# Kernel optimization log

Measured on AMD Instinct MI355X. Metric: run time of the kernel, lower is better.

The kernel has to match this reference:

```python
import jax, jax.numpy as jnp
import numpy as np

B, S, D, H, BLK, R = 2, 4096, 768, 12, 64, 3
NB = S // BLK  # 64 blocks
HD = D // H    # 64 head dim


def layer_norm(x, g, b, eps=1e-6):
    m = jnp.mean(x, -1, keepdims=True)
    v = jnp.mean((x - m) ** 2, -1, keepdims=True)
    return (x - m) / jnp.sqrt(v + eps) * g + b


def bigbird_attention(x, wq, bq, wk, bk, wv, bv, wo, bo, rand_attn):
    # x: [B,S,D]; rand_attn: [H, NB-2, R] int block indices
    def heads(t):
        return t.reshape(B, S, H, HD).transpose(0, 2, 1, 3)  # [B,H,S,HD]
    q = heads(x @ wq + bq)
    k = heads(x @ wk + bk)
    v = heads(x @ wv + bv)
    scale = 1.0 / jnp.sqrt(jnp.asarray(HD, x.dtype))

    qb = q.reshape(B, H, NB, BLK, HD)
    kb = k.reshape(B, H, NB, BLK, HD)
    vb = v.reshape(B, H, NB, BLK, HD)

    # --- global query blocks (first & last) attend to the full sequence ---
    qg = jnp.concatenate([qb[:, :, :1], qb[:, :, -1:]], axis=2)  # [B,H,2,BLK,HD]
    sg = jnp.einsum('bhnqd,bhkd->bhnqk', qg, k) * scale          # [B,H,2,BLK,S]
    og = jnp.einsum('bhnqk,bhkd->bhnqd', jax.nn.softmax(sg, -1), v)

    # --- middle query blocks: global(2) + window(3) + random(R) key blocks ---
    mids = jnp.arange(1, NB - 1)                                  # [NB-2]
    win = jnp.stack([mids - 1, mids, mids + 1], -1)               # [NB-2,3]
    glb = jnp.broadcast_to(jnp.array([0, NB - 1]), (NB - 2, 2))   # [NB-2,2]
    fixed = jnp.concatenate([glb, win], -1)                       # [NB-2,5]
    idx = jnp.concatenate(
        [jnp.broadcast_to(fixed, (H, NB - 2, 5)), rand_attn], -1)  # [H,NB-2,5+R]
    h_ix = jnp.arange(H)[:, None, None]
    km = kb[:, h_ix, idx].reshape(B, H, NB - 2, (5 + R) * BLK, HD)
    vm = vb[:, h_ix, idx].reshape(B, H, NB - 2, (5 + R) * BLK, HD)
    sm = jnp.einsum('bhnqd,bhnkd->bhnqk', qb[:, :, 1:-1], km) * scale
    om = jnp.einsum('bhnqk,bhnkd->bhnqd', jax.nn.softmax(sm, -1), vm)

    ob = jnp.concatenate([og[:, :, :1], om, og[:, :, 1:]], axis=2)  # [B,H,NB,BLK,HD]
    out = ob.reshape(B, H, S, HD).transpose(0, 2, 1, 3).reshape(B, S, D)
    return out @ wo + bo


def mlp(x, w1, b1, w2, b2):
    return jax.nn.gelu(x @ w1 + b1) @ w2 + b2


def setup_inputs() -> dict:
    key = jax.random.key(0)
    ks = jax.random.split(key, 8)
    s = 0.02
    return {
        'x': jax.random.normal(ks[0], (B, S, D, 2), jnp.float32),
        'ln1_g': jnp.ones((D,), jnp.float32),
        'ln1_b': jnp.zeros((D,), jnp.float32),
        'ln2_g': jnp.ones((D,), jnp.float32),
        'ln2_b': jnp.zeros((D,), jnp.float32),
        'wq': jax.random.normal(ks[1], (D, D), jnp.float32) * s,
        'bq': jnp.zeros((D,), jnp.float32),
        'wk': jax.random.normal(ks[2], (D, D), jnp.float32) * s,
        'bk': jnp.zeros((D,), jnp.float32),
        'wv': jax.random.normal(ks[3], (D, D), jnp.float32) * s,
        'bv': jnp.zeros((D,), jnp.float32),
        'wo': jax.random.normal(ks[4], (D, D), jnp.float32) * s,
        'bo': jnp.zeros((D,), jnp.float32),
        'w1': jax.random.normal(ks[5], (D, 4 * D), jnp.float32) * s,
        'b1': jnp.zeros((4 * D,), jnp.float32),
        'w2': jax.random.normal(ks[6], (4 * D, D), jnp.float32) * s,
        'b2': jnp.zeros((D,), jnp.float32),
        'rand_attn': jax.random.randint(ks[7], (H, NB - 2, R), 1, NB - 1),
    }


def reference(x, ln1_g, ln1_b, ln2_g, ln2_b, wq, bq, wk, bk, wv, bv, wo, bo,
              w1, b1, w2, b2, rand_attn):
    # x: [B,S,D,2]; chunk(2,-1): first chunk -> x2, second -> x1
    x2 = x[..., 0]
    x1 = x[..., 1]
    y2 = x2 + bigbird_attention(layer_norm(x1, ln1_g, ln1_b),
                                wq, bq, wk, bk, wv, bv, wo, bo, rand_attn)
    y1 = x1 + mlp(layer_norm(y2, ln2_g, ln2_b), w1, b1, w2, b2)
    return jnp.stack([y1, y2], axis=-1)  # cat([y1,y2], -1)
```

## Files before the change

kernel.cpp:

```cpp
#include <hip/hip_runtime.h>
#include <cstdint>
#include <cstddef>

typedef __attribute__((ext_vector_type(8))) short bfr8;
typedef __attribute__((ext_vector_type(4))) float acc4;

__device__ __forceinline__ float bf2f(short s) {
  return __uint_as_float(((unsigned)(unsigned short)s) << 16);
}
__device__ __forceinline__ short f2bf(float f) {
  unsigned u = __float_as_uint(f);
  u += 0x7fffu + ((u >> 16) & 1u);
  return (short)(u >> 16);
}
__device__ __forceinline__ float gelu_f(float x) {
  float z = 0.7978845608028654f * (x + 0.044715f * x * x * x);
  z = fminf(fmaxf(z, -12.f), 12.f);
  float e = __expf(2.f * z);
  float th = (e - 1.f) / (e + 1.f);
  return 0.5f * x * (1.f + th);
}
__device__ __forceinline__ void load_lds16(const short* g, short* l) {
  __builtin_amdgcn_global_load_lds(
      (const __attribute__((address_space(1))) void*)g,
      (__attribute__((address_space(3))) void*)l, 16, 0, 0);
}

#define BB 2
#define SS 4096
#define DD 768
#define HH 12
#define BLKSZ 64
#define NBLK 64
#define HDIM 64

__global__ __launch_bounds__(256) void prep_weights(
    const float* __restrict__ wq, const float* __restrict__ wk,
    const float* __restrict__ wv, const float* __restrict__ wo,
    const float* __restrict__ w1, const float* __restrict__ w2,
    const float* __restrict__ bq, const float* __restrict__ bk,
    const float* __restrict__ bv, float* __restrict__ bqkv,
    short* __restrict__ wqT, short* __restrict__ wkT, short* __restrict__ wvT,
    short* __restrict__ woT, short* __restrict__ w1T, short* __restrict__ w2T) {
  int id = blockIdx.x;
  if (id >= 6912) {
    int t = (id - 6912) * 256 + threadIdx.x;
    bqkv[t] = (t < 768) ? bq[t] : (t < 1536) ? bk[t - 768] : bv[t - 1536];
    return;
  }
  const float* src; short* dst; int K, N, n0, k0;
  if (id < 2304) {
    int seg = id / 576, local = id % 576;
    K = 768; N = 768;
    n0 = (local % 24) * 32; k0 = (local / 24) * 32;
    src = seg == 0 ? wq : seg == 1 ? wk : seg == 2 ? wv : wo;
    dst = seg == 0 ? wqT : seg == 1 ? wkT : seg == 2 ? wvT : woT;
  } else if (id < 4608) {
    int local = id - 2304;
    K = 768; N = 3072;
    n0 = (local % 96) * 32; k0 = (local / 96) * 32;
    src = w1; dst = w1T;
  } else {
    int local = id - 4608;
    K = 3072; N = 768;
    n0 = (local % 24) * 32; k0 = (local / 24) * 32;
    src = w2; dst = w2T;
  }
  __shared__ float tile[32][33];
  int tx = threadIdx.x & 31, ty = threadIdx.x >> 5;
#pragma unroll
  for (int i = 0; i < 4; i++) {
    int kk = ty + i * 8;
    tile[kk][tx] = src[(size_t)(k0 + kk) * N + n0 + tx];
  }
  __syncthreads();
#pragma unroll
  for (int i = 0; i < 4; i++) {
    int nn = ty + i * 8;
    dst[(size_t)(n0 + nn) * K + k0 + tx] = f2bf(tile[tx][nn]);
  }
}

__global__ __launch_bounds__(256) void transpose_bf16(
    const short* __restrict__ src, short* __restrict__ dst) {
  __shared__ short tile[32][33];
  int b = blockIdx.z;
  int s0 = blockIdx.x * 32, d0 = blockIdx.y * 32;
  int tx = threadIdx.x & 31, ty = threadIdx.x >> 5;
#pragma unroll
  for (int i = 0; i < 4; i++) {
    int ss = ty + i * 8;
    tile[ss][tx] = src[((size_t)b * SS + s0 + ss) * DD + d0 + tx];
  }
  __syncthreads();
#pragma unroll
  for (int i = 0; i < 4; i++) {
    int dd = ty + i * 8;
    dst[((size_t)b * DD + d0 + dd) * SS + s0 + tx] = tile[tx][dd];
  }
}

__global__ __launch_bounds__(256) void ln_kernel(
    const float* __restrict__ in, int stride, int off,
    const float* __restrict__ gam, const float* __restrict__ bet,
    short* __restrict__ out) {
  int row = blockIdx.x;
  int t = threadIdx.x;
  const float* base = in + (size_t)row * 768 * stride + off;
  float vals[3], s = 0.f, s2 = 0.f;
#pragma unroll
  for (int i = 0; i < 3; i++) {
    int d = t + 256 * i;
    float v = base[(size_t)d * stride];
    vals[i] = v; s += v; s2 += v * v;
  }
#pragma unroll
  for (int o = 32; o; o >>= 1) { s += __shfl_down(s, o); s2 += __shfl_down(s2, o); }
  __shared__ float red[8];
  int lane = t & 63, w = t >> 6;
  if (lane == 0) { red[w] = s; red[4 + w] = s2; }
  __syncthreads();
  s = red[0] + red[1] + red[2] + red[3];
  s2 = red[4] + red[5] + red[6] + red[7];
  float mean = s * (1.f / 768.f);
  float var = s2 * (1.f / 768.f) - mean * mean;
  float rstd = rsqrtf(var + 1e-6f);
#pragma unroll
  for (int i = 0; i < 3; i++) {
    int d = t + 256 * i;
    out[(size_t)row * 768 + d] = f2bf((vals[i] - mean) * rstd * gam[d] + bet[d]);
  }
}

template <int BM, int BN, int EPI>
__global__ __launch_bounds__(256) void gemm_lds(
    const short* __restrict__ A, const short* __restrict__ BT,
    const float* __restrict__ bias, const float* __restrict__ xres,
    const float* __restrict__ aux, void* __restrict__ outp, int M, int N, int K) {
  __shared__ alignas(16) short As[BM * 64];
  __shared__ alignas(16) short Bs[BN * 64];
  constexpr int TI = BM / 32;
  constexpr int TJ = BN / 32;
  int m0 = blockIdx.y * BM, n0 = blockIdx.x * BN;
  int t = threadIdx.x;
  int lane = t & 63, wave = t >> 6;
  int wm = (wave >> 1) * (BM / 2), wn = (wave & 1) * (BN / 2);
  int quad = lane >> 4, lc = lane & 15;
  acc4 acc[TI][TJ];
#pragma unroll
  for (int i = 0; i < TI; i++)
#pragma unroll
    for (int j = 0; j < TJ; j++) acc[i][j] = (acc4){0.f, 0.f, 0.f, 0.f};

  int aflat = wave * (BM * 16) + lane * 8;
  const short* Ag = A + (size_t)(m0 + (aflat >> 6)) * K + (aflat & 63);
  int bflat = wave * (BN * 16) + lane * 8;
  const short* Bg = BT + (size_t)(n0 + (bflat >> 6)) * K + (bflat & 63);

  for (int k0 = 0; k0 < K; k0 += 64) {
#pragma unroll
    for (int j = 0; j < TI; j++)
      load_lds16(Ag + k0 + (size_t)(j * 8) * K, &As[wave * (BM * 16) + j * 512]);
#pragma unroll
    for (int j = 0; j < TJ; j++)
      load_lds16(Bg + k0 + (size_t)(j * 8) * K, &Bs[wave * (BN * 16) + j * 512]);
    __syncthreads();
#pragma unroll
    for (int kk = 0; kk < 2; kk++) {
      int kof = kk * 32 + quad * 8;
      bfr8 afr[TI], bfr[TJ];
#pragma unroll
      for (int i = 0; i < TI; i++) afr[i] = *(const bfr8*)&As[(wm + i * 16 + lc) * 64 + kof];
#pragma unroll
      for (int j = 0; j < TJ; j++) bfr[j] = *(const bfr8*)&Bs[(wn + j * 16 + lc) * 64 + kof];
#pragma unroll
      for (int i = 0; i < TI; i++)
#pragma unroll
        for (int j = 0; j < TJ; j++)
          acc[i][j] = __builtin_amdgcn_mfma_f32_16x16x32_bf16(afr[i], bfr[j], acc[i][j], 0, 0, 0);
    }
    __syncthreads();
  }
#pragma unroll
  for (int i = 0; i < TI; i++) {
#pragma unroll
    for (int j = 0; j < TJ; j++) {
      int col = n0 + wn + j * 16 + lc;
      float bv = bias[col];
#pragma unroll
      for (int r = 0; r < 4; r++) {
        int row = m0 + wm + i * 16 + quad * 4 + r;
        float v = acc[i][j][r] + bv;
        size_t idx = (size_t)row * N + col;
        if (EPI == 1) {
          v += xres[idx * 2];
          ((float*)outp)[idx * 2 + 1] = v;
        } else if (EPI == 2) {
          ((short*)outp)[idx] = f2bf(gelu_f(v));
        } else if (EPI == 3) {
          v += xres[idx * 2 + 1];
          ((float*)outp)[idx * 2] = v;
        } else if (EPI == 4) {
          int bufidx = col / 768;
          int colm = col - bufidx * 768;
          ((short*)outp)[(size_t)bufidx * 6291456 + (size_t)row * 768 + colm] = f2bf(v);
        } else if (EPI == 5) {
          v += xres[idx * 2];
          ((float*)outp)[idx] = v;
        } else {
          v += xres[idx * 2 + 1];
          float2 pr; pr.x = v; pr.y = aux[idx];
          ((float2*)outp)[idx] = pr;
        }
      }
    }
  }
}

__device__ __forceinline__ void attn_core(
    const short* __restrict__ qrow0, const short* __restrict__ kbase,
    const short* __restrict__ vt_h, const int* kblist, int nch, int t,
    short (*QPs)[72], short (*Ks)[72], short (*Vts)[72],
    float* m, float* l, acc4* O) {
  int lane = t & 63, w = t >> 6, quad = lane >> 4, lc = lane & 15;
#pragma unroll
  for (int c = t; c < 512; c += 256) {
    int r = c >> 3, dc = c & 7;
    *(bfr8*)&QPs[r][dc * 8] = *(const bfr8*)&qrow0[(size_t)r * DD + dc * 8];
  }
  __syncthreads();
  bfr8 aq0 = *(const bfr8*)&QPs[w * 16 + lc][quad * 8];
  bfr8 aq1 = *(const bfr8*)&QPs[w * 16 + lc][32 + quad * 8];
#pragma unroll
  for (int r = 0; r < 4; r++) { m[r] = -1e30f; l[r] = 0.f; }
#pragma unroll
  for (int dt = 0; dt < 4; dt++) O[dt] = (acc4){0.f, 0.f, 0.f, 0.f};

  for (int ch = 0; ch < nch; ch++) {
    int kb = kblist[ch];
    __syncthreads();
#pragma unroll
    for (int c = t; c < 512; c += 256) {
      int r = c >> 3, dc = c & 7;
      *(bfr8*)&Ks[r][dc * 8] = *(const bfr8*)&kbase[((size_t)kb * 64 + r) * DD + dc * 8];
      *(bfr8*)&Vts[r][dc * 8] = *(const bfr8*)&vt_h[(size_t)r * SS + kb * 64 + dc * 8];
    }
    __syncthreads();
    acc4 sacc[4];
#pragma unroll
    for (int nt = 0; nt < 4; nt++) {
      bfr8 bk0 = *(const bfr8*)&Ks[nt * 16 + lc][quad * 8];
      bfr8 bk1 = *(const bfr8*)&Ks[nt * 16 + lc][32 + quad * 8];
      acc4 z = (acc4){0.f, 0.f, 0.f, 0.f};
      z = __builtin_amdgcn_mfma_f32_16x16x32_bf16(aq0, bk0, z, 0, 0, 0);
      z = __builtin_amdgcn_mfma_f32_16x16x32_bf16(aq1, bk1, z, 0, 0, 0);
      sacc[nt] = z;
    }
#pragma unroll
    for (int r = 0; r < 4; r++) {
      float sv[4];
#pragma unroll
      for (int nt = 0; nt < 4; nt++) sv[nt] = sacc[nt][r] * 0.125f;
      float cm = fmaxf(fmaxf(sv[0], sv[1]), fmaxf(sv[2], sv[3]));
      cm = fmaxf(cm, __shfl_xor(cm, 1));
      cm = fmaxf(cm, __shfl_xor(cm, 2));
      cm = fmaxf(cm, __shfl_xor(cm, 4));
      cm = fmaxf(cm, __shfl_xor(cm, 8));
      float mn = fmaxf(m[r], cm);
      float al = __expf(m[r] - mn);
      m[r] = mn;
      float ls = 0.f;
#pragma unroll
      for (int nt = 0; nt < 4; nt++) {
        float p = __expf(sv[nt] - mn);
        ls += p;
        QPs[w * 16 + quad * 4 + r][nt * 16 + lc] = f2bf(p);
      }
      ls += __shfl_xor(ls, 1);
      ls += __shfl_xor(ls, 2);
      ls += __shfl_xor(ls, 4);
      ls += __shfl_xor(ls, 8);
      l[r] = l[r] * al + ls;
#pragma unroll
      for (int dt = 0; dt < 4; dt++) O[dt][r] *= al;
    }
    bfr8 ap0 = *(const bfr8*)&QPs[w * 16 + lc][quad * 8];
    bfr8 ap1 = *(const bfr8*)&QPs[w * 16 + lc][32 + quad * 8];
#pragma unroll
    for (int dt = 0; dt < 4; dt++) {
      bfr8 bv0 = *(const bfr8*)&Vts[dt * 16 + lc][quad * 8];
      bfr8 bv1 = *(const bfr8*)&Vts[dt * 16 + lc][32 + quad * 8];
      O[dt] = __builtin_amdgcn_mfma_f32_16x16x32_bf16(ap0, bv0, O[dt], 0, 0, 0);
      O[dt] = __builtin_amdgcn_mfma_f32_16x16x32_bf16(ap1, bv1, O[dt], 0, 0, 0);
    }
  }
}

__global__ __launch_bounds__(256) void attn_mid_mfma(
    const short* __restrict__ qbuf, const short* __restrict__ kbuf,
    const short* __restrict__ vtbuf, const int* __restrict__ rand_attn,
    short* __restrict__ ao) {
  int n = 1 + blockIdx.x;
  int h = blockIdx.y, b = blockIdx.z;
  int t = threadIdx.x, lane = t & 63, w = t >> 6, quad = lane >> 4, lc = lane & 15;
  int hoff = h * HDIM;
  size_t btok = (size_t)b * SS;
  __shared__ alignas(16) short QPs[64][72], Ks[64][72], Vts[64][72];
  int kblist[8];
  kblist[0] = 0; kblist[1] = NBLK - 1;
  kblist[2] = n - 1; kblist[3] = n; kblist[4] = n + 1;
#pragma unroll
  for (int r = 0; r < 3; r++)
    kblist[5 + r] = rand_attn[((size_t)h * 62 + (n - 1)) * 3 + r];
  float m[4], l[4]; acc4 O[4];
  attn_core(qbuf + (btok + (size_t)n * 64) * DD + hoff,
            kbuf + btok * DD + hoff,
            vtbuf + ((size_t)b * DD + hoff) * SS,
            kblist, 8, t, QPs, Ks, Vts, m, l, O);
#pragma unroll
  for (int r = 0; r < 4; r++) {
    float inv = 1.f / l[r];
    size_t tok = btok + (size_t)n * 64 + w * 16 + quad * 4 + r;
    short* op = ao + tok * DD + hoff;
#pragma unroll
    for (int dt = 0; dt < 4; dt++) op[dt * 16 + lc] = f2bf(O[dt][r] * inv);
  }
}

__global__ __launch_bounds__(256) void attn_glb_mfma(
    const short* __restrict__ qbuf, const short* __restrict__ kbuf,
    const short* __restrict__ vtbuf, float* __restrict__ part) {
  int g = blockIdx.x & 1, s = blockIdx.x >> 1;
  int h = blockIdx.y, b = blockIdx.z;
  int t = threadIdx.x, lane = t & 63, w = t >> 6, quad = lane >> 4, lc = lane & 15;
  int hoff = h * HDIM;
  size_t btok = (size_t)b * SS;
  int qblk = g ? (NBLK - 1) : 0;
  __shared__ alignas(16) short QPs[64][72], Ks[64][72], Vts[64][72];
  int kblist[8];
#pragma unroll
  for (int c = 0; c < 8; c++) kblist[c] = s * 8 + c;
  float m[4], l[4]; acc4 O[4];
  attn_core(qbuf + (btok + (size_t)qblk * 64) * DD + hoff,
            kbuf + btok * DD + hoff,
            vtbuf + ((size_t)b * DD + hoff) * SS,
            kblist, 8, t, QPs, Ks, Vts, m, l, O);
  float* pp = part + ((((size_t)b * HH + h) * 2 + g) * 8 + s) * 4224;
#pragma unroll
  for (int r = 0; r < 4; r++) {
    int row = w * 16 + quad * 4 + r;
#pragma unroll
    for (int dt = 0; dt < 4; dt++) pp[row * 64 + dt * 16 + lc] = O[dt][r];
    if (lc == 0) {
      pp[4096 + row] = m[r];
      pp[4160 + row] = l[r];
    }
  }
}

__global__ __launch_bounds__(256) void attn_combine(
    const float* __restrict__ part, short* __restrict__ ao) {
  int g = blockIdx.x, h = blockIdx.y, b = blockIdx.z;
  int t = threadIdx.x, qrow = t >> 2, sub = t & 3;
  const float* base = part + (((size_t)b * HH + h) * 2 + g) * 8 * 4224;
  float mm[8], ll[8], M = -1e30f;
#pragma unroll
  for (int s = 0; s < 8; s++) {
    mm[s] = base[s * 4224 + 4096 + qrow];
    ll[s] = base[s * 4224 + 4160 + qrow];
    M = fmaxf(M, mm[s]);
  }
  float L = 0.f, O[16];
#pragma unroll
  for (int d = 0; d < 16; d++) O[d] = 0.f;
#pragma unroll
  for (int s = 0; s < 8; s++) {
    float w = __expf(mm[s] - M);
    L += w * ll[s];
    const float* Op = base + s * 4224 + qrow * 64 + sub * 16;
#pragma unroll
    for (int d = 0; d < 16; d++) O[d] += w * Op[d];
  }
  float inv = 1.f / L;
  int qblk = g ? (NBLK - 1) : 0;
  size_t tok = (size_t)b * SS + (size_t)qblk * BLKSZ + qrow;
  short* op = ao + tok * DD + h * HDIM + sub * 16;
#pragma unroll
  for (int d = 0; d < 16; d++) op[d] = f2bf(O[d] * inv);
}

extern "C" void kernel_launch(void* const* d_in, const int* in_sizes, int n_in,
                              void* d_out, int out_size, void* d_ws, size_t ws_size,
                              hipStream_t stream) {
  (void)in_sizes; (void)n_in; (void)out_size;
  const float* x     = (const float*)d_in[0];
  const float* ln1_g = (const float*)d_in[1];
  const float* ln1_b = (const float*)d_in[2];
  const float* ln2_g = (const float*)d_in[3];
  const float* ln2_b = (const float*)d_in[4];
  const float* wq = (const float*)d_in[5];
  const float* bq = (const float*)d_in[6];
  const float* wk = (const float*)d_in[7];
  const float* bk = (const float*)d_in[8];
  const float* wv = (const float*)d_in[9];
  const float* bv = (const float*)d_in[10];
  const float* wo = (const float*)d_in[11];
  const float* bo = (const float*)d_in[12];
  const float* w1 = (const float*)d_in[13];
  const float* b1 = (const float*)d_in[14];
  const float* w2 = (const float*)d_in[15];
  const float* b2 = (const float*)d_in[16];
  const int* rand_attn = (const int*)d_in[17];
  float* out = (float*)d_out;

  short* wsb = (short*)d_ws;
  const size_t WD = 589824;
  const size_t WB = 2359296;
  const size_t ACT = 6291456;
  short* wqT = wsb;
  short* wkT = wqT + WD;
  short* wvT = wkT + WD;
  short* woT = wvT + WD;
  short* w1T = woT + WD;
  short* w2T = w1T + WB;
  short* xln = w2T + WB;
  short* qb  = xln + ACT;
  short* kb  = qb + ACT;
  short* vb  = kb + ACT;
  short* aob = vb + ACT;
  float* partp = (float*)(aob + ACT);
  float* bqkv = partp + 1622016;
  float* y2f  = bqkv + 2304;
  short* vbT = xln;
  short* h1 = xln;
  short* ln2b = aob;

  const size_t NEED = ((size_t)(y2f + ACT) - (size_t)d_ws);
  bool big = ws_size >= NEED;

  prep_weights<<<6921, 256, 0, stream>>>(wq, wk, wv, wo, w1, w2, bq, bk, bv, bqkv,
                                         wqT, wkT, wvT, woT, w1T, w2T);

  ln_kernel<<<8192, 256, 0, stream>>>(x, 2, 1, ln1_g, ln1_b, xln);

  gemm_lds<64, 128, 4><<<dim3(18, 128), 256, 0, stream>>>(
      xln, wqT, bqkv, nullptr, nullptr, qb, 8192, 2304, 768);

  transpose_bf16<<<dim3(128, 24, 2), 256, 0, stream>>>(vb, vbT);

  attn_mid_mfma<<<dim3(62, 12, 2), 256, 0, stream>>>(qb, kb, vbT, rand_attn, aob);
  attn_glb_mfma<<<dim3(16, 12, 2), 256, 0, stream>>>(qb, kb, vbT, partp);
  attn_combine<<<dim3(2, 12, 2), 256, 0, stream>>>(partp, aob);

  if (big) {
    gemm_lds<64, 128, 5><<<dim3(6, 128), 256, 0, stream>>>(
        aob, woT, bo, x, nullptr, y2f, 8192, 768, 768);
    ln_kernel<<<8192, 256, 0, stream>>>(y2f, 1, 0, ln2_g, ln2_b, ln2b);
    gemm_lds<64, 128, 2><<<dim3(24, 128), 256, 0, stream>>>(
        ln2b, w1T, b1, nullptr, nullptr, h1, 8192, 3072, 768);
    gemm_lds<64, 128, 6><<<dim3(6, 128), 256, 0, stream>>>(
        h1, w2T, b2, x, y2f, out, 8192, 768, 3072);
  } else {
    gemm_lds<64, 128, 1><<<dim3(6, 128), 256, 0, stream>>>(
        aob, woT, bo, x, nullptr, out, 8192, 768, 768);
    ln_kernel<<<8192, 256, 0, stream>>>((const float*)d_out, 2, 1, ln2_g, ln2_b, ln2b);
    gemm_lds<64, 128, 2><<<dim3(24, 128), 256, 0, stream>>>(
        ln2b, w1T, b1, nullptr, nullptr, h1, 8192, 3072, 768);
    gemm_lds<64, 128, 3><<<dim3(6, 128), 256, 0, stream>>>(
        h1, w2T, b2, x, nullptr, out, 8192, 768, 3072);
  }
}
```

Measured before the change: 472.9 us.

## Replace GEMM with 256-row tiled, double-buffered, 8-phase pipelined MFMA kernel

Swaps the simple 64x128 single-buffered LDS GEMM for a 256xBN tile kernel with 512 threads. It double-buffers A and B in swizzled LDS and interleaves async global-to-LDS loads with MFMA phases, using explicit waitcnt, barriers and priority hints. The kernel also remaps block IDs so each XCD works on contiguous M chunks for better L2 reuse. The aim is to hide memory latency and raise MFMA utilisation in the projection and MLP GEMMs, which dominate runtime. In exchange it needs large dynamic LDS (up to 128KB), launches fewer blocks, and depends on fragile hand-tuned vmcnt counts.

```diff
diff --git a/kernel.cpp b/kernel.cpp
--- a/kernel.cpp
+++ b/kernel.cpp
@@ -132,59 +132,122 @@
   }
 }
 
-template <int BM, int BN, int EPI>
-__global__ __launch_bounds__(256) void gemm_lds(
+template <int BN, int EPI, int SWZ>
+__global__ __launch_bounds__(512, 2) void gemm_8ph(
     const short* __restrict__ A, const short* __restrict__ BT,
     const float* __restrict__ bias, const float* __restrict__ xres,
     const float* __restrict__ aux, void* __restrict__ outp, int M, int N, int K) {
-  __shared__ alignas(16) short As[BM * 64];
-  __shared__ alignas(16) short Bs[BN * 64];
-  constexpr int TI = BM / 32;
-  constexpr int TJ = BN / 32;
-  int m0 = blockIdx.y * BM, n0 = blockIdx.x * BN;
-  int t = threadIdx.x;
-  int lane = t & 63, wave = t >> 6;
-  int wm = (wave >> 1) * (BM / 2), wn = (wave & 1) * (BN / 2);
-  int quad = lane >> 4, lc = lane & 15;
-  acc4 acc[TI][TJ];
-#pragma unroll
-  for (int i = 0; i < TI; i++)
-#pragma unroll
-    for (int j = 0; j < TJ; j++) acc[i][j] = (acc4){0.f, 0.f, 0.f, 0.f};
-
-  int aflat = wave * (BM * 16) + lane * 8;
-  const short* Ag = A + (size_t)(m0 + (aflat >> 6)) * K + (aflat & 63);
-  int bflat = wave * (BN * 16) + lane * 8;
-  const short* Bg = BT + (size_t)(n0 + (bflat >> 6)) * K + (bflat & 63);
-
-  for (int k0 = 0; k0 < K; k0 += 64) {
-#pragma unroll
-    for (int j = 0; j < TI; j++)
-      load_lds16(Ag + k0 + (size_t)(j * 8) * K, &As[wave * (BM * 16) + j * 512]);
-#pragma unroll
-    for (int j = 0; j < TJ; j++)
-      load_lds16(Bg + k0 + (size_t)(j * 8) * K, &Bs[wave * (BN * 16) + j * 512]);
-    __syncthreads();
-#pragma unroll
-    for (int kk = 0; kk < 2; kk++) {
-      int kof = kk * 32 + quad * 8;
-      bfr8 afr[TI], bfr[TJ];
-#pragma unroll
-      for (int i = 0; i < TI; i++) afr[i] = *(const bfr8*)&As[(wm + i * 16 + lc) * 64 + kof];
-#pragma unroll
-      for (int j = 0; j < TJ; j++) bfr[j] = *(const bfr8*)&Bs[(wn + j * 16 + lc) * 64 + kof];
-#pragma unroll
-      for (int i = 0; i < TI; i++)
-#pragma unroll
-        for (int j = 0; j < TJ; j++)
-          acc[i][j] = __builtin_amdgcn_mfma_f32_16x16x32_bf16(afr[i], bfr[j], acc[i][j], 0, 0, 0);
-    }
-    __syncthreads();
-  }
-#pragma unroll
-  for (int i = 0; i < TI; i++) {
-#pragma unroll
-    for (int j = 0; j < TJ; j++) {
+  constexpr int NJ = BN / 64;
+  constexpr int NJ2 = NJ / 2;
+  constexpr int LB = BN / 128;
+  extern __shared__ short lds[];
+  int gx = gridDim.x;
+  int orig = blockIdx.x + gx * blockIdx.y;
+  int mchunk = gridDim.y >> 3;
+  int xcd = orig & 7, l = orig >> 3;
+  int mb, nb;
+  if (SWZ == 0) { nb = l / mchunk; mb = xcd * mchunk + (l % mchunk); }
+  else          { nb = l % gx;     mb = xcd * mchunk + (l / gx); }
+  int m0 = mb * 256, n0 = nb * BN;
+  const int t = threadIdx.x;
+  const int lane = t & 63, wave = t >> 6;
+  const int wm = (wave >> 2) * 128;
+  const int wn = (wave & 3) * (BN / 4);
+  const int quad = lane >> 4, lc = lane & 15;
+  const int rsw = (lc & 7) << 4;
+
+  const int srow = t >> 3;
+  const int sg = ((t & 7) ^ (srow & 7)) * 8;
+  const short* Asrc = A + (size_t)(m0 + srow) * K + sg;
+  const short* Bsrc = BT + (size_t)(n0 + srow) * K + sg;
+
+  acc4 acc[8][NJ];
+#pragma unroll
+  for (int i = 0; i < 8; i++)
+#pragma unroll
+    for (int j = 0; j < NJ; j++) acc[i][j] = (acc4){0.f, 0.f, 0.f, 0.f};
+  bfr8 a0[4][2], a1[4][2], b0[NJ2][2], b1[NJ2][2];
+
+#define SA_(buf, half, c, kt) load_lds16(Asrc + ((size_t)((half)*128 + (c)*64)) * K + (size_t)(kt) * 64, \
+                                         lds + (buf)*16384 + ((half)*128 + (c)*64)*64 + t*8)
+#define SB_(buf, half, c, kt) load_lds16(Bsrc + ((size_t)((half)*(BN/2) + (c)*64)) * K + (size_t)(kt) * 64, \
+                                         lds + 32768 + (buf)*(BN*64) + ((half)*(BN/2) + (c)*64)*64 + t*8)
+#define SAH(buf, half, kt) do { SA_(buf, half, 0, kt); SA_(buf, half, 1, kt); } while (0)
+#define SBH(buf, half, kt) do { SB_(buf, half, 0, kt); if (LB == 2) SB_(buf, half, 1, kt); } while (0)
+#define RA_(arr, buf, half) \
+  _Pragma("unroll") for (int i_ = 0; i_ < 4; i_++) \
+  _Pragma("unroll") for (int k_ = 0; k_ < 2; k_++) \
+    arr[i_][k_] = *(const bfr8*)((const char*)lds + (buf)*32768 + \
+        (wm + (half)*64 + i_*16 + lc)*128 + (((k_<<6)|(quad<<4)) ^ rsw))
+#define RB_(arr, buf, half) \
+  _Pragma("unroll") for (int j_ = 0; j_ < NJ2; j_++) \
+  _Pragma("unroll") for (int k_ = 0; k_ < 2; k_++) \
+    arr[j_][k_] = *(const bfr8*)((const char*)lds + 65536 + (buf)*(BN*128) + \
+        (wn + (half)*(NJ2*16) + j_*16 + lc)*128 + (((k_<<6)|(quad<<4)) ^ rsw))
+#define MM_(aarr, barr, i0, j0) \
+  _Pragma("unroll") for (int i_ = 0; i_ < 4; i_++) \
+  _Pragma("unroll") for (int j_ = 0; j_ < NJ2; j_++) \
+  _Pragma("unroll") for (int k_ = 0; k_ < 2; k_++) \
+    acc[(i0)+i_][(j0)+j_] = __builtin_amdgcn_mfma_f32_16x16x32_bf16( \
+        aarr[i_][k_], barr[j_][k_], acc[(i0)+i_][(j0)+j_], 0, 0, 0)
+#define SB0_ __builtin_amdgcn_sched_barrier(0)
+#define BAR_ __builtin_amdgcn_s_barrier()
+#define PH_OPEN do { SB0_; BAR_; \
+    asm volatile("s_waitcnt lgkmcnt(0)" ::: "memory"); SB0_; \
+    __builtin_amdgcn_s_setprio(1); } while (0)
+#define PH_CLOSE do { __builtin_amdgcn_s_setprio(0); SB0_; } while (0)
+#define VM_CNT do { if constexpr (LB == 2) asm volatile("s_waitcnt vmcnt(4)" ::: "memory"); \
+                    else                   asm volatile("s_waitcnt vmcnt(3)" ::: "memory"); \
+                    SB0_; } while (0)
+#define VM_ZERO do { asm volatile("s_waitcnt vmcnt(0)" ::: "memory"); SB0_; } while (0)
+
+  const int nk = K >> 6;
+  SAH(0, 0, 0); SAH(0, 1, 0); SBH(0, 0, 0); SBH(0, 1, 0);
+  SBH(1, 0, 1); SAH(1, 0, 1);
+  VM_CNT;
+  BAR_;
+
+  for (int it = 0; it < nk; it += 2) {
+    const bool more = (it + 2) < nk;
+    RA_(a0, 0, 0); RB_(b0, 0, 0); SAH(1, 1, it + 1);
+    PH_OPEN; MM_(a0, b0, 0, 0); PH_CLOSE; BAR_;
+    RB_(b1, 0, 1); SBH(1, 1, it + 1);
+    PH_OPEN; MM_(a0, b1, 0, NJ2); PH_CLOSE; BAR_;
+    RA_(a1, 0, 1); if (more) SBH(0, 0, it + 2);
+    PH_OPEN; MM_(a1, b0, 4, 0); PH_CLOSE; BAR_;
+    if (more) SAH(0, 0, it + 2);
+    PH_OPEN; MM_(a1, b1, 4, NJ2); PH_CLOSE;
+    if (more) { VM_CNT; } else { VM_ZERO; }
+    BAR_;
+    RA_(a0, 1, 0); RB_(b0, 1, 0); if (more) SAH(0, 1, it + 2);
+    PH_OPEN; MM_(a0, b0, 0, 0); PH_CLOSE; BAR_;
+    RB_(b1, 1, 1); if (more) SBH(0, 1, it + 2);
+    PH_OPEN; MM_(a0, b1, 0, NJ2); PH_CLOSE; BAR_;
+    RA_(a1, 1, 1); if (more) SBH(1, 0, it + 3);
+    PH_OPEN; MM_(a1, b0, 4, 0); PH_CLOSE; BAR_;
+    if (more) SAH(1, 0, it + 3);
+    PH_OPEN; MM_(a1, b1, 4, NJ2); PH_CLOSE;
+    if (more) { VM_CNT; }
+    BAR_;
+  }
+#undef SA_
+#undef SB_
+#undef SAH
+#undef SBH
+#undef RA_
+#undef RB_
+#undef MM_
+#undef PH_OPEN
+#undef PH_CLOSE
+#undef VM_CNT
+#undef VM_ZERO
+#undef SB0_
+#undef BAR_
+
+#pragma unroll
+  for (int i = 0; i < 8; i++) {
+#pragma unroll
+    for (int j = 0; j < NJ; j++) {
       int col = n0 + wn + j * 16 + lc;
       float bv = bias[col];
 #pragma unroll
@@ -438,12 +501,15 @@
   const size_t NEED = ((size_t)(y2f + ACT) - (size_t)d_ws);
   bool big = ws_size >= NEED;
 
+  const size_t LDS_256 = 131072;
+  const size_t LDS_128 = 98304;
+
   prep_weights<<<6921, 256, 0, stream>>>(wq, wk, wv, wo, w1, w2, bq, bk, bv, bqkv,
                                          wqT, wkT, wvT, woT, w1T, w2T);
 
   ln_kernel<<<8192, 256, 0, stream>>>(x, 2, 1, ln1_g, ln1_b, xln);
 
-  gemm_lds<64, 128, 4><<<dim3(18, 128), 256, 0, stream>>>(
+  gemm_8ph<256, 4, 0><<<dim3(9, 32), 512, LDS_256, stream>>>(
       xln, wqT, bqkv, nullptr, nullptr, qb, 8192, 2304, 768);
 
   transpose_bf16<<<dim3(128, 24, 2), 256, 0, stream>>>(vb, vbT);
@@ -453,20 +519,20 @@
   attn_combine<<<dim3(2, 12, 2), 256, 0, stream>>>(partp, aob);
 
   if (big) {
-    gemm_lds<64, 128, 5><<<dim3(6, 128), 256, 0, stream>>>(
+    gemm_8ph<128, 5, 0><<<dim3(6, 32), 512, LDS_128, stream>>>(
         aob, woT, bo, x, nullptr, y2f, 8192, 768, 768);
     ln_kernel<<<8192, 256, 0, stream>>>(y2f, 1, 0, ln2_g, ln2_b, ln2b);
-    gemm_lds<64, 128, 2><<<dim3(24, 128), 256, 0, stream>>>(
+    gemm_8ph<256, 2, 0><<<dim3(12, 32), 512, LDS_256, stream>>>(
         ln2b, w1T, b1, nullptr, nullptr, h1, 8192, 3072, 768);
-    gemm_lds<64, 128, 6><<<dim3(6, 128), 256, 0, stream>>>(
+    gemm_8ph<128, 6, 1><<<dim3(6, 32), 512, LDS_128, stream>>>(
         h1, w2T, b2, x, y2f, out, 8192, 768, 3072);
   } else {
-    gemm_lds<64, 128, 1><<<dim3(6, 128), 256, 0, stream>>>(
+    gemm_8ph<128, 1, 0><<<dim3(6, 32), 512, LDS_128, stream>>>(
         aob, woT, bo, x, nullptr, out, 8192, 768, 768);
     ln_kernel<<<8192, 256, 0, stream>>>((const float*)d_out, 2, 1, ln2_g, ln2_b, ln2b);
-    gemm_lds<64, 128, 2><<<dim3(24, 128), 256, 0, stream>>>(
+    gemm_8ph<256, 2, 0><<<dim3(12, 32), 512, LDS_256, stream>>>(
         ln2b, w1T, b1, nullptr, nullptr, h1, 8192, 3072, 768);
-    gemm_lds<64, 128, 3><<<dim3(6, 128), 256, 0, stream>>>(
+    gemm_8ph<128, 3, 1><<<dim3(6, 32), 512, LDS_128, stream>>>(
         h1, w2T, b2, x, nullptr, out, 8192, 768, 3072);
   }
 }
```

Measured after the change: 451.9 us. 4.4% less time.
